# Kernel tuning notes

Measured on AMD Instinct MI355X. Metric: run time of the kernel, lower is better.

Reference implementation:

```python
import jax, jax.numpy as jnp
import numpy as np

NUM_GROUPS = 8
EPS = 1e-5


def group_norm(x, gamma, beta):
    # x: [B, C, H, W]
    B, C, H, W = x.shape
    xg = x.reshape(B, NUM_GROUPS, C // NUM_GROUPS, H, W)
    mean = xg.mean(axis=(2, 3, 4), keepdims=True)
    var = xg.var(axis=(2, 3, 4), keepdims=True)
    xn = ((xg - mean) * jax.lax.rsqrt(var + EPS)).reshape(B, C, H, W)
    return xn * gamma[None, :, None, None] + beta[None, :, None, None]


def conv1x1(x, w, b):
    # x: [B, C, H, W], w: [Cout, Cin], b: [Cout]
    return jnp.einsum('bchw,oc->bohw', x, w) + b[None, :, None, None]


def setup_inputs() -> dict:
    key = jax.random.key(0)
    ks = jax.random.split(key, 7)
    C = 128
    x = jax.random.normal(ks[0], (4, C, 64, 64), dtype=jnp.float32)
    norm_w = jnp.ones((C,), dtype=jnp.float32)
    norm_b = jnp.zeros((C,), dtype=jnp.float32)
    s = 1.0 / np.sqrt(C)
    qkv_w = jax.random.normal(ks[1], (3 * C, C), dtype=jnp.float32) * s
    qkv_b = jax.random.normal(ks[2], (3 * C,), dtype=jnp.float32) * 0.01
    proj_w = jax.random.normal(ks[3], (C, C), dtype=jnp.float32) * s
    proj_b = jax.random.normal(ks[4], (C,), dtype=jnp.float32) * 0.01
    return {"x": x, "norm_w": norm_w, "norm_b": norm_b,
            "qkv_w": qkv_w, "qkv_b": qkv_b,
            "proj_w": proj_w, "proj_b": proj_b}


def reference(x, norm_w, norm_b, qkv_w, qkv_b, proj_w, proj_b):
    B, C, H, W = x.shape
    qkv = conv1x1(group_norm(x, norm_w, norm_b), qkv_w, qkv_b)
    q, k, v = jnp.split(qkv, 3, axis=1)           # each [B, C, H, W]
    q = q.reshape(B, C, H * W).transpose(0, 2, 1)  # [B, HW, C]
    k = k.reshape(B, C, H * W)                     # [B, C, HW]
    v = v.reshape(B, C, H * W).transpose(0, 2, 1)  # [B, HW, C]
    scale = 1.0 / np.sqrt(C).astype(np.float32)
    attn = jax.nn.softmax(jnp.einsum('bnc,bcm->bnm', q, k) * scale, axis=-1)
    out = jnp.einsum('bnm,bmc->bnc', attn, v)      # [B, HW, C]
    out = out.transpose(0, 2, 1).reshape(B, C, H, W)
    return x + conv1x1(out, proj_w, proj_b)
```

## Files before the change

### kernel.cpp

```cpp
#include <hip/hip_runtime.h>

typedef unsigned short u16;
typedef unsigned int   u32;

#define HW 4096
#define NC 128

typedef __bf16 bf16x8 __attribute__((ext_vector_type(8)));
typedef float  f32x16 __attribute__((ext_vector_type(16)));

__device__ __forceinline__ bf16x8 as_bf8(uint4 u){
    union { uint4 u; bf16x8 b; } c; c.u = u; return c.b;
}
__device__ __forceinline__ u16 f2bf(float f){
    u32 u = __float_as_uint(f);
    return (u16)((u + 0x7fffu + ((u >> 16) & 1u)) >> 16);
}
__device__ __forceinline__ u32 pack2(float a, float b){
    return ((__float_as_uint(a) + 0x8000u) >> 16) | ((__float_as_uint(b) + 0x8000u) & 0xffff0000u);
}
__device__ __forceinline__ float bf_lo(u32 u){ return __uint_as_float(u << 16); }
__device__ __forceinline__ float bf_hi(u32 u){ return __uint_as_float(u & 0xffff0000u); }
__device__ __forceinline__ void unpack8(uint4 u, float* v){
    v[0]=bf_lo(u.x); v[1]=bf_hi(u.x); v[2]=bf_lo(u.y); v[3]=bf_hi(u.y);
    v[4]=bf_lo(u.z); v[5]=bf_hi(u.z); v[6]=bf_lo(u.w); v[7]=bf_hi(u.w);
}

__device__ __forceinline__ float exp2_hw(float x){ return __builtin_amdgcn_exp2f(x); }

__device__ __forceinline__ void plswap(u32 &a, u32 &b){
    asm("v_permlane32_swap_b32 %0, %1" : "+v"(a), "+v"(b));
}
__device__ __forceinline__ u32 cvtpk(float a, float b){
    u32 r; asm("v_cvt_pk_bf16_f32 %0, %1, %2" : "=v"(r) : "v"(a), "v"(b)); return r;
}

__global__ __launch_bounds__(256) void gnw_kernel(const float* __restrict__ x,
                                                  float* __restrict__ stats,
                                                  const float* __restrict__ qkv_w,
                                                  const float* __restrict__ proj_w,
                                                  uint4* __restrict__ Wf,
                                                  uint4* __restrict__ Pf){
    if (blockIdx.x < 256){
        int bg = blockIdx.x >> 3, part = blockIdx.x & 7;
        const float4* p = (const float4*)(x + (size_t)bg * 65536 + part * 8192);
        float s = 0.f, ss = 0.f;
        #pragma unroll
        for (int i = 0; i < 8; i++){
            float4 u = p[threadIdx.x + i*256];
            s  += u.x + u.y + u.z + u.w;
            ss += u.x*u.x + u.y*u.y + u.z*u.z + u.w*u.w;
        }
        #pragma unroll
        for (int off = 32; off > 0; off >>= 1){
            s  += __shfl_xor(s,  off);
            ss += __shfl_xor(ss, off);
        }
        __shared__ float rs[4], rss[4];
        int wid = threadIdx.x >> 6;
        if ((threadIdx.x & 63) == 0){ rs[wid] = s; rss[wid] = ss; }
        __syncthreads();
        if (threadIdx.x == 0){
            stats[bg*16 + part*2]     = rs[0]+rs[1]+rs[2]+rs[3];
            stats[bg*16 + part*2 + 1] = rss[0]+rss[1]+rss[2]+rss[3];
        }
    } else {
        int id = (blockIdx.x - 256)*256 + threadIdx.x;
        const float* src; uint4* dst; int fi;
        if (id < 6144){ src = qkv_w; dst = Wf; fi = id; }
        else          { src = proj_w; dst = Pf; fi = id - 6144; }
        int l = fi & 63, ks = (fi >> 6) & 7, ob = fi >> 9;
        int o = ob*32 + (l & 31);
        int c = ks*16 + ((l >> 5) << 3);
        const float* s = src + o*128 + c;
        dst[fi] = make_uint4(pack2(s[0],s[1]), pack2(s[2],s[3]), pack2(s[4],s[5]), pack2(s[6],s[7]));
    }
}

__global__ __launch_bounds__(256) void qkv_kernel(const float* __restrict__ x,
                                                  const float* __restrict__ stats,
                                                  const float* __restrict__ gamma,
                                                  const float* __restrict__ beta,
                                                  const uint4* __restrict__ Wf,
                                                  const float* __restrict__ bias,
                                                  uint4* __restrict__ Qf,
                                                  uint4* __restrict__ Kf,
                                                  uint4* __restrict__ Vf){
    __shared__ float gaL[128], beL[128], biasL[384];
    int b = blockIdx.x >> 7, tokblk = blockIdx.x & 127;
    int t = threadIdx.x, lane = t & 63, wv = t >> 6;
    if (t < 128){
        int g = t >> 4;
        float S = 0.f, SS = 0.f;
        #pragma unroll
        for (int p = 0; p < 8; p++){
            S  += stats[(b*8 + g)*16 + p*2];
            SS += stats[(b*8 + g)*16 + p*2 + 1];
        }
        float mean = S * (1.f/65536.f);
        float rstd = rsqrtf(SS * (1.f/65536.f) - mean*mean + 1e-5f);
        float ga = gamma[t] * rstd;
        gaL[t] = ga; beL[t] = beta[t] - mean*ga;
    }
    if (t < 192){ biasL[t] = bias[t]; biasL[t+192] = bias[t+192]; }
    __syncthreads();

    int h = lane >> 5, tl = lane & 31;
    uint4 xf[8];
    const float* xb = x + (size_t)b*128*HW + tokblk*32 + tl;
    #pragma unroll
    for (int ks = 0; ks < 8; ks++){
        int c0 = ks*16 + h*8;
        float4 g0 = *(float4*)&gaL[c0], g1 = *(float4*)&gaL[c0+4];
        float4 e0 = *(float4*)&beL[c0], e1 = *(float4*)&beL[c0+4];
        float v[8];
        #pragma unroll
        for (int j = 0; j < 8; j++) v[j] = xb[(size_t)(c0+j)*HW];
        v[0] = fmaf(v[0], g0.x, e0.x); v[1] = fmaf(v[1], g0.y, e0.y);
        v[2] = fmaf(v[2], g0.z, e0.z); v[3] = fmaf(v[3], g0.w, e0.w);
        v[4] = fmaf(v[4], g1.x, e1.x); v[5] = fmaf(v[5], g1.y, e1.y);
        v[6] = fmaf(v[6], g1.z, e1.z); v[7] = fmaf(v[7], g1.w, e1.w);
        xf[ks] = make_uint4(pack2(v[0],v[1]), pack2(v[2],v[3]), pack2(v[4],v[5]), pack2(v[6],v[7]));
    }

    bool up = (lane >= 32);
    #pragma unroll
    for (int i = 0; i < 3; i++){
        int ob = wv*3 + i;
        uint4 wf[8];
        #pragma unroll
        for (int ks = 0; ks < 8; ks++) wf[ks] = Wf[(ob*8 + ks)*64 + lane];
        f32x16 D;
        #pragma unroll
        for (int r = 0; r < 16; r++) D[r] = 0.f;
        if (ob < 8){
            #pragma unroll
            for (int ks = 0; ks < 8; ks++)
                D = __builtin_amdgcn_mfma_f32_32x32x16_bf16(as_bf8(wf[ks]), as_bf8(xf[ks]), D, 0,0,0);
            #pragma unroll
            for (int r = 0; r < 16; r++)
                D[r] += biasL[ob*32 + (r&3) + 8*(r>>2) + 4*h];
            u32 pk[8], xch[8];
            #pragma unroll
            for (int j = 0; j < 8; j++) pk[j] = pack2(D[2*j], D[2*j+1]);
            #pragma unroll
            for (int j = 0; j < 8; j++) xch[j] = __shfl_xor(pk[j], 32);
            uint4 F0 = up ? make_uint4(xch[2],xch[3],pk[2],pk[3]) : make_uint4(pk[0],pk[1],xch[0],xch[1]);
            uint4 F1 = up ? make_uint4(xch[6],xch[7],pk[6],pk[7]) : make_uint4(pk[4],pk[5],xch[4],xch[5]);
            uint4* dst = (ob < 4) ? Qf : Kf;
            int obl = ob & 3;
            size_t base = (((size_t)b*128 + tokblk)*8 + obl*2)*64 + lane;
            dst[base] = F0; dst[base + 64] = F1;
        } else {
            #pragma unroll
            for (int ks = 0; ks < 8; ks++)
                D = __builtin_amdgcn_mfma_f32_32x32x16_bf16(as_bf8(xf[ks]), as_bf8(wf[ks]), D, 0,0,0);
            int nb = ob - 8;
            float vb = biasL[256 + nb*32 + tl];
            #pragma unroll
            for (int r = 0; r < 16; r++) D[r] += vb;
            u32 pk[8], xch[8];
            #pragma unroll
            for (int j = 0; j < 8; j++) pk[j] = pack2(D[2*j], D[2*j+1]);
            #pragma unroll
            for (int j = 0; j < 8; j++) xch[j] = __shfl_xor(pk[j], 32);
            uint4 F0 = up ? make_uint4(xch[2],xch[3],pk[2],pk[3]) : make_uint4(pk[0],pk[1],xch[0],xch[1]);
            uint4 F1 = up ? make_uint4(xch[6],xch[7],pk[6],pk[7]) : make_uint4(pk[4],pk[5],xch[4],xch[5]);
            int it = tokblk >> 1, t2 = tokblk & 1;
            size_t base = ((((size_t)b*64 + it)*4 + nb)*4 + t2*2)*64 + lane;
            Vf[base] = F0; Vf[base + 64] = F1;
        }
    }
}

__global__ __launch_bounds__(256, 2) void attn_kernel(const uint4* __restrict__ Qf,
                                                      const uint4* __restrict__ Kf,
                                                      const uint4* __restrict__ Vf,
                                                      uint4* __restrict__ Opart,
                                                      float* __restrict__ lsum){
    __shared__ float fsm[8192];
    __shared__ float lred[64];
    int pair = blockIdx.x & 7, qx = blockIdx.x >> 3;
    int b = pair >> 1, ksp = pair & 1;
    int t = threadIdx.x, lane = t & 63, wv = t >> 6;
    int qh = wv >> 1, kh = wv & 1;
    const float SC2 = 0.12751744361402804f;
    const float B2  = -11.541560327111707f;

    uint4 qf[8];
    const uint4* qptr = Qf + (((size_t)b*128 + qx*2 + qh)*8)*64 + lane;
    #pragma unroll
    for (int ks = 0; ks < 8; ks++) qf[ks] = qptr[ks*64];

    f32x16 O[4];
    #pragma unroll
    for (int nb = 0; nb < 4; nb++)
        #pragma unroll
        for (int r = 0; r < 16; r++) O[nb][r] = 0.f;
    float l_i = 0.f;

    const uint4* kgw = Kf + (((size_t)b*128 + ksp*64)*8)*64 + (kh<<9) + lane;
    const uint4* vgw = Vf + (((size_t)b*64  + ksp*32)*16)*64 + (kh<<7) + lane;

    uint4 kf[8], vf[8];
    #pragma unroll
    for (int ks = 0; ks < 8; ks++) kf[ks] = kgw[ks*64];
    #pragma unroll
    for (int nb = 0; nb < 4; nb++){
        vf[nb*2]   = vgw[nb*256];
        vf[nb*2+1] = vgw[nb*256 + 64];
    }

    for (int it = 0; it < 32; it++){
        f32x16 Sa, Sb;
        #pragma unroll
        for (int r = 0; r < 16; r++){ Sa[r] = 0.f; Sb[r] = 0.f; }
        #pragma unroll
        for (int ks = 0; ks < 4; ks++)
            Sa = __builtin_amdgcn_mfma_f32_32x32x16_bf16(as_bf8(kf[ks]), as_bf8(qf[ks]), Sa, 0,0,0);
        #pragma unroll
        for (int ks = 4; ks < 8; ks++)
            Sb = __builtin_amdgcn_mfma_f32_32x32x16_bf16(as_bf8(kf[ks]), as_bf8(qf[ks]), Sb, 0,0,0);
        #pragma unroll
        for (int r = 0; r < 16; r++) Sa[r] += Sb[r];

        if (it < 31){
            const uint4* kn = kgw + (it+1)*1024;
            #pragma unroll
            for (int ks = 0; ks < 8; ks++) kf[ks] = kn[ks*64];
        }

        float psum = 0.f;
        u32 pk[8];
        #pragma unroll
        for (int q = 0; q < 4; q++){
            float e0 = exp2_hw(__fmaf_rn(Sa[q*4+0], SC2, B2));
            float e1 = exp2_hw(__fmaf_rn(Sa[q*4+1], SC2, B2));
            float e2 = exp2_hw(__fmaf_rn(Sa[q*4+2], SC2, B2));
            float e3 = exp2_hw(__fmaf_rn(Sa[q*4+3], SC2, B2));
            psum += (e0+e1)+(e2+e3);
            pk[2*q] = cvtpk(e0,e1); pk[2*q+1] = cvtpk(e2,e3);
        }
        {
            u32 ua = __float_as_uint(psum), ub = ua;
            plswap(ua, ub);
            l_i += __uint_as_float(ua) + __uint_as_float(ub);
        }

        plswap(pk[0], pk[2]); plswap(pk[1], pk[3]);
        plswap(pk[4], pk[6]); plswap(pk[5], pk[7]);
        uint4 fr0 = make_uint4(pk[0], pk[1], pk[2], pk[3]);
        uint4 fr1 = make_uint4(pk[4], pk[5], pk[6], pk[7]);

        #pragma unroll
        for (int nb = 0; nb < 4; nb++){
            O[nb] = __builtin_amdgcn_mfma_f32_32x32x16_bf16(as_bf8(vf[nb*2]),   as_bf8(fr0), O[nb], 0,0,0);
            O[nb] = __builtin_amdgcn_mfma_f32_32x32x16_bf16(as_bf8(vf[nb*2+1]), as_bf8(fr1), O[nb], 0,0,0);
        }

        if (it < 31){
            const uint4* vn = vgw + (it+1)*1024;
            #pragma unroll
            for (int nb = 0; nb < 4; nb++){
                vf[nb*2]   = vn[nb*256];
                vf[nb*2+1] = vn[nb*256 + 64];
            }
        }
    }

    if (kh == 1){
        #pragma unroll
        for (int nb = 0; nb < 4; nb++)
            #pragma unroll
            for (int r = 0; r < 16; r++)
                fsm[((qh*4+nb)*16 + r)*64 + lane] = O[nb][r];
        if (lane < 32) lred[qh*32 + lane] = l_i;
    }
    __syncthreads();
    if (kh == 0){
        float lt = l_i + lred[qh*32 + (lane & 31)];
        if (lane < 32) lsum[((size_t)(ksp*4 + b))*HW + (qx*2+qh)*32 + lane] = lt;
        bool up = (lane >= 32);
        uint4* oc = Opart + (size_t)ksp*262144 + (((size_t)b*128 + qx*2 + qh)*8)*64 + lane;
        #pragma unroll
        for (int nb = 0; nb < 4; nb++){
            #pragma unroll
            for (int r = 0; r < 16; r++) O[nb][r] += fsm[((qh*4+nb)*16 + r)*64 + lane];
            u32 pk[8], xch[8];
            #pragma unroll
            for (int j = 0; j < 8; j++) pk[j] = pack2(O[nb][2*j], O[nb][2*j+1]);
            #pragma unroll
            for (int j = 0; j < 8; j++) xch[j] = __shfl_xor(pk[j], 32);
            uint4 F0 = up ? make_uint4(xch[2],xch[3],pk[2],pk[3]) : make_uint4(pk[0],pk[1],xch[0],xch[1]);
            uint4 F1 = up ? make_uint4(xch[6],xch[7],pk[6],pk[7]) : make_uint4(pk[4],pk[5],xch[4],xch[5]);
            oc[(nb*2)*64]     = F0;
            oc[(nb*2 + 1)*64] = F1;
        }
    }
}

__global__ __launch_bounds__(256) void proj_kernel(const uint4* __restrict__ Op,
                                                   const float* __restrict__ lsum,
                                                   const uint4* __restrict__ Pf,
                                                   const float* __restrict__ bias,
                                                   const float* __restrict__ x,
                                                   float* __restrict__ out){
    __shared__ float biasL[128];
    int t = threadIdx.x, lane = t & 63, wv = t >> 6;
    if (t < 128) biasL[t] = bias[t];
    __syncthreads();
    int b = blockIdx.x >> 6, tk = blockIdx.x & 63;
    int tokb2 = wv & 1, obh = wv >> 1;
    int tokblk = tk*2 + tokb2;
    int h = lane >> 5, tl = lane & 31;

    int rowg = b*HW + tokblk*32 + tl;
    float inv = 1.f / (lsum[rowg] + lsum[16384 + rowg]);
    const uint4* c0p = Op + (((size_t)b*128 + tokblk)*8)*64 + lane;
    uint4 af[8];
    #pragma unroll
    for (int ks = 0; ks < 8; ks++){
        uint4 u0 = c0p[ks*64];
        uint4 u1 = c0p[262144 + ks*64];
        float v0[8], v1[8];
        unpack8(u0, v0); unpack8(u1, v1);
        u32 q[4];
        #pragma unroll
        for (int j = 0; j < 4; j++)
            q[j] = pack2((v0[2*j] + v1[2*j]) * inv, (v0[2*j+1] + v1[2*j+1]) * inv);
        af[ks] = make_uint4(q[0], q[1], q[2], q[3]);
    }

    #pragma unroll
    for (int i = 0; i < 2; i++){
        int ob = obh*2 + i;
        uint4 pf[8];
        #pragma unroll
        for (int ks = 0; ks < 8; ks++) pf[ks] = Pf[(ob*8 + ks)*64 + lane];
        f32x16 D;
        #pragma unroll
        for (int r = 0; r < 16; r++) D[r] = 0.f;
        #pragma unroll
        for (int ks = 0; ks < 8; ks++)
            D = __builtin_amdgcn_mfma_f32_32x32x16_bf16(as_bf8(pf[ks]), as_bf8(af[ks]), D, 0,0,0);
        #pragma unroll
        for (int r = 0; r < 16; r++){
            int o = ob*32 + (r&3) + 8*(r>>2) + 4*h;
            size_t gi = ((size_t)b*128 + o)*HW + tokblk*32 + tl;
            out[gi] = x[gi] + biasL[o] + D[r];
        }
    }
}

extern "C" void kernel_launch(void* const* d_in, const int* in_sizes, int n_in,
                              void* d_out, int out_size, void* d_ws, size_t ws_size,
                              hipStream_t stream){
    const float* x      = (const float*)d_in[0];
    const float* norm_w = (const float*)d_in[1];
    const float* norm_b = (const float*)d_in[2];
    const float* qkv_w  = (const float*)d_in[3];
    const float* qkv_b  = (const float*)d_in[4];
    const float* proj_w = (const float*)d_in[5];
    const float* proj_b = (const float*)d_in[6];
    float* out = (float*)d_out;

    char* w = (char*)d_ws;
    float* stats = (float*)w;
    uint4* Qf = (uint4*)(w + 2048);
    uint4* Kf = (uint4*)(w + 2048 + 4194304);
    uint4* Vf = (uint4*)(w + 2048 + 8388608);
    float* lsum = (float*)(w + 2048 + 12582912);
    uint4* Wf = (uint4*)(w + 2048 + 12582912 + 131072);
    uint4* Pf = (uint4*)(w + 2048 + 12582912 + 131072 + 98304);
    uint4* Opart = (uint4*)d_out;

    gnw_kernel<<<288, 256, 0, stream>>>(x, stats, qkv_w, proj_w, Wf, Pf);
    qkv_kernel<<<512, 256, 0, stream>>>(x, stats, norm_w, norm_b, Wf, qkv_b, Qf, Kf, Vf);
    attn_kernel<<<512, 256, 0, stream>>>(Qf, Kf, Vf, Opart, lsum);
    proj_kernel<<<256, 256, 0, stream>>>(Opart, lsum, Pf, proj_b, x, out);
}
```

Measured before the change: 130.8 us.

## Split attention keys four ways and fold partial-output merge into projection MFMAs

Templates the attention kernel on the number of key splits and, when the workspace is large enough, uses four splits with 1024 blocks, writing partial outputs to a workspace buffer. A new projection kernel sums the four unnormalized partials through MFMA accumulation (linearity of the projection) and applies the softmax normalizer afterward. This replaces the explicit bf16 unpack/add/repack. The aim is more parallelism in attention and less combine overhead. The cost is extra partial-output traffic and more projection MFMAs, and the old two-split path is kept as a fallback for small workspaces.

```diff
diff --git a/kernel.cpp b/kernel.cpp
--- a/kernel.cpp
+++ b/kernel.cpp
@@ -12,19 +12,11 @@
 __device__ __forceinline__ bf16x8 as_bf8(uint4 u){
     union { uint4 u; bf16x8 b; } c; c.u = u; return c.b;
 }
-__device__ __forceinline__ u16 f2bf(float f){
-    u32 u = __float_as_uint(f);
-    return (u16)((u + 0x7fffu + ((u >> 16) & 1u)) >> 16);
-}
 __device__ __forceinline__ u32 pack2(float a, float b){
     return ((__float_as_uint(a) + 0x8000u) >> 16) | ((__float_as_uint(b) + 0x8000u) & 0xffff0000u);
 }
 __device__ __forceinline__ float bf_lo(u32 u){ return __uint_as_float(u << 16); }
 __device__ __forceinline__ float bf_hi(u32 u){ return __uint_as_float(u & 0xffff0000u); }
-__device__ __forceinline__ void unpack8(uint4 u, float* v){
-    v[0]=bf_lo(u.x); v[1]=bf_hi(u.x); v[2]=bf_lo(u.y); v[3]=bf_hi(u.y);
-    v[4]=bf_lo(u.z); v[5]=bf_hi(u.z); v[6]=bf_lo(u.w); v[7]=bf_hi(u.w);
-}
 
 __device__ __forceinline__ float exp2_hw(float x){ return __builtin_amdgcn_exp2f(x); }
 
@@ -173,15 +165,18 @@
     }
 }
 
+template<int NS>
 __global__ __launch_bounds__(256, 2) void attn_kernel(const uint4* __restrict__ Qf,
                                                       const uint4* __restrict__ Kf,
                                                       const uint4* __restrict__ Vf,
                                                       uint4* __restrict__ Opart,
                                                       float* __restrict__ lsum){
+    constexpr int ITERS = 64 / NS;
+    constexpr int PB    = (NS == 2) ? 3 : 4;
     __shared__ float fsm[8192];
     __shared__ float lred[64];
-    int pair = blockIdx.x & 7, qx = blockIdx.x >> 3;
-    int b = pair >> 1, ksp = pair & 1;
+    int pair = blockIdx.x & ((1 << PB) - 1), qx = blockIdx.x >> PB;
+    int b = pair >> (PB - 2), ksp = pair & (NS - 1);
     int t = threadIdx.x, lane = t & 63, wv = t >> 6;
     int qh = wv >> 1, kh = wv & 1;
     const float SC2 = 0.12751744361402804f;
@@ -199,8 +194,8 @@
         for (int r = 0; r < 16; r++) O[nb][r] = 0.f;
     float l_i = 0.f;
 
-    const uint4* kgw = Kf + (((size_t)b*128 + ksp*64)*8)*64 + (kh<<9) + lane;
-    const uint4* vgw = Vf + (((size_t)b*64  + ksp*32)*16)*64 + (kh<<7) + lane;
+    const uint4* kgw = Kf + (((size_t)b*128 + ksp*(128/NS))*8)*64 + (kh<<9) + lane;
+    const uint4* vgw = Vf + (((size_t)b*64  + ksp*(64/NS))*16)*64 + (kh<<7) + lane;
 
     uint4 kf[8], vf[8];
     #pragma unroll
@@ -211,7 +206,7 @@
         vf[nb*2+1] = vgw[nb*256 + 64];
     }
 
-    for (int it = 0; it < 32; it++){
+    for (int it = 0; it < ITERS; it++){
         f32x16 Sa, Sb;
         #pragma unroll
         for (int r = 0; r < 16; r++){ Sa[r] = 0.f; Sb[r] = 0.f; }
@@ -224,7 +219,7 @@
         #pragma unroll
         for (int r = 0; r < 16; r++) Sa[r] += Sb[r];
 
-        if (it < 31){
+        if (it < ITERS-1){
             const uint4* kn = kgw + (it+1)*1024;
             #pragma unroll
             for (int ks = 0; ks < 8; ks++) kf[ks] = kn[ks*64];
@@ -258,7 +253,7 @@
             O[nb] = __builtin_amdgcn_mfma_f32_32x32x16_bf16(as_bf8(vf[nb*2+1]), as_bf8(fr1), O[nb], 0,0,0);
         }
 
-        if (it < 31){
+        if (it < ITERS-1){
             const uint4* vn = vgw + (it+1)*1024;
             #pragma unroll
             for (int nb = 0; nb < 4; nb++){
@@ -299,12 +294,12 @@
     }
 }
 
-__global__ __launch_bounds__(256) void proj_kernel(const uint4* __restrict__ Op,
-                                                   const float* __restrict__ lsum,
-                                                   const uint4* __restrict__ Pf,
-                                                   const float* __restrict__ bias,
-                                                   const float* __restrict__ x,
-                                                   float* __restrict__ out){
+__global__ __launch_bounds__(256) void proj2_kernel(const uint4* __restrict__ Op,
+                                                    const float* __restrict__ lsum,
+                                                    const uint4* __restrict__ Pf,
+                                                    const float* __restrict__ bias,
+                                                    const float* __restrict__ x,
+                                                    float* __restrict__ out){
     __shared__ float biasL[128];
     int t = threadIdx.x, lane = t & 63, wv = t >> 6;
     if (t < 128) biasL[t] = bias[t];
@@ -317,18 +312,11 @@
     int rowg = b*HW + tokblk*32 + tl;
     float inv = 1.f / (lsum[rowg] + lsum[16384 + rowg]);
     const uint4* c0p = Op + (((size_t)b*128 + tokblk)*8)*64 + lane;
-    uint4 af[8];
+    uint4 of0[8], of1[8];
     #pragma unroll
     for (int ks = 0; ks < 8; ks++){
-        uint4 u0 = c0p[ks*64];
-        uint4 u1 = c0p[262144 + ks*64];
-        float v0[8], v1[8];
-        unpack8(u0, v0); unpack8(u1, v1);
-        u32 q[4];
-        #pragma unroll
-        for (int j = 0; j < 4; j++)
-            q[j] = pack2((v0[2*j] + v1[2*j]) * inv, (v0[2*j+1] + v1[2*j+1]) * inv);
-        af[ks] = make_uint4(q[0], q[1], q[2], q[3]);
+        of0[ks] = c0p[ks*64];
+        of1[ks] = c0p[262144 + ks*64];
     }
 
     #pragma unroll
@@ -342,13 +330,60 @@
         for (int r = 0; r < 16; r++) D[r] = 0.f;
         #pragma unroll
         for (int ks = 0; ks < 8; ks++)
-            D = __builtin_amdgcn_mfma_f32_32x32x16_bf16(as_bf8(pf[ks]), as_bf8(af[ks]), D, 0,0,0);
+            D = __builtin_amdgcn_mfma_f32_32x32x16_bf16(as_bf8(pf[ks]), as_bf8(of0[ks]), D, 0,0,0);
+        #pragma unroll
+        for (int ks = 0; ks < 8; ks++)
+            D = __builtin_amdgcn_mfma_f32_32x32x16_bf16(as_bf8(pf[ks]), as_bf8(of1[ks]), D, 0,0,0);
         #pragma unroll
         for (int r = 0; r < 16; r++){
             int o = ob*32 + (r&3) + 8*(r>>2) + 4*h;
             size_t gi = ((size_t)b*128 + o)*HW + tokblk*32 + tl;
-            out[gi] = x[gi] + biasL[o] + D[r];
-        }
+            out[gi] = x[gi] + biasL[o] + D[r]*inv;
+        }
+    }
+}
+
+__global__ __launch_bounds__(256) void proj4_kernel(const uint4* __restrict__ Op,
+                                                    const float* __restrict__ lsum,
+                                                    const uint4* __restrict__ Pf,
+                                                    const float* __restrict__ bias,
+                                                    const float* __restrict__ x,
+                                                    float* __restrict__ out){
+    __shared__ float biasL[128];
+    int t = threadIdx.x, lane = t & 63, ob = t >> 6;
+    if (t < 128) biasL[t] = bias[t];
+    __syncthreads();
+    int b = blockIdx.x >> 7, tokblk = blockIdx.x & 127;
+    int h = lane >> 5, tl = lane & 31;
+    int tok = tokblk*32 + tl;
+
+    float ls = 0.f;
+    #pragma unroll
+    for (int p = 0; p < 4; p++) ls += lsum[((size_t)(p*4 + b))*HW + tok];
+    float inv = 1.f / ls;
+
+    uint4 pf[8];
+    #pragma unroll
+    for (int ks = 0; ks < 8; ks++) pf[ks] = Pf[(ob*8 + ks)*64 + lane];
+
+    const uint4* cp = Op + (((size_t)b*128 + tokblk)*8)*64 + lane;
+    f32x16 D;
+    #pragma unroll
+    for (int r = 0; r < 16; r++) D[r] = 0.f;
+    #pragma unroll
+    for (int c = 0; c < 4; c++){
+        uint4 of[8];
+        #pragma unroll
+        for (int ks = 0; ks < 8; ks++) of[ks] = cp[(size_t)c*262144 + ks*64];
+        #pragma unroll
+        for (int ks = 0; ks < 8; ks++)
+            D = __builtin_amdgcn_mfma_f32_32x32x16_bf16(as_bf8(pf[ks]), as_bf8(of[ks]), D, 0,0,0);
+    }
+    #pragma unroll
+    for (int r = 0; r < 16; r++){
+        int o = ob*32 + (r&3) + 8*(r>>2) + 4*h;
+        size_t gi = ((size_t)b*128 + o)*HW + tokblk*32 + tl;
+        out[gi] = x[gi] + biasL[o] + D[r]*inv;
     }
 }
 
@@ -363,19 +398,36 @@
     const float* proj_w = (const float*)d_in[5];
     const float* proj_b = (const float*)d_in[6];
     float* out = (float*)d_out;
-
     char* w = (char*)d_ws;
-    float* stats = (float*)w;
-    uint4* Qf = (uint4*)(w + 2048);
-    uint4* Kf = (uint4*)(w + 2048 + 4194304);
-    uint4* Vf = (uint4*)(w + 2048 + 8388608);
-    float* lsum = (float*)(w + 2048 + 12582912);
-    uint4* Wf = (uint4*)(w + 2048 + 12582912 + 131072);
-    uint4* Pf = (uint4*)(w + 2048 + 12582912 + 131072 + 98304);
-    uint4* Opart = (uint4*)d_out;
-
-    gnw_kernel<<<288, 256, 0, stream>>>(x, stats, qkv_w, proj_w, Wf, Pf);
-    qkv_kernel<<<512, 256, 0, stream>>>(x, stats, norm_w, norm_b, Wf, qkv_b, Qf, Kf, Vf);
-    attn_kernel<<<512, 256, 0, stream>>>(Qf, Kf, Vf, Opart, lsum);
-    proj_kernel<<<256, 256, 0, stream>>>(Opart, lsum, Pf, proj_b, x, out);
-}
+
+    const size_t needA = 2048 + 3*4194304 + 262144 + 98304 + 32768 + 16777216;
+    if (ws_size >= needA){
+        float* stats = (float*)w;
+        uint4* Qf   = (uint4*)(w + 2048);
+        uint4* Kf   = (uint4*)(w + 2048 + 4194304);
+        uint4* Vf   = (uint4*)(w + 2048 + 8388608);
+        float* lsum = (float*)(w + 12584960);
+        uint4* Wf   = (uint4*)(w + 12847104);
+        uint4* Pf   = (uint4*)(w + 12945408);
+        uint4* Op4  = (uint4*)(w + 12978176);
+
+        gnw_kernel<<<288, 256, 0, stream>>>(x, stats, qkv_w, proj_w, Wf, Pf);
+        qkv_kernel<<<512, 256, 0, stream>>>(x, stats, norm_w, norm_b, Wf, qkv_b, Qf, Kf, Vf);
+        attn_kernel<4><<<1024, 256, 0, stream>>>(Qf, Kf, Vf, Op4, lsum);
+        proj4_kernel<<<512, 256, 0, stream>>>(Op4, lsum, Pf, proj_b, x, out);
+    } else {
+        float* stats = (float*)w;
+        uint4* Qf   = (uint4*)(w + 2048);
+        uint4* Kf   = (uint4*)(w + 2048 + 4194304);
+        uint4* Vf   = (uint4*)(w + 2048 + 8388608);
+        float* lsum = (float*)(w + 2048 + 12582912);
+        uint4* Wf   = (uint4*)(w + 2048 + 12582912 + 131072);
+        uint4* Pf   = (uint4*)(w + 2048 + 12582912 + 131072 + 98304);
+        uint4* Opart = (uint4*)d_out;
+
+        gnw_kernel<<<288, 256, 0, stream>>>(x, stats, qkv_w, proj_w, Wf, Pf);
+        qkv_kernel<<<512, 256, 0, stream>>>(x, stats, norm_w, norm_b, Wf, qkv_b, Qf, Kf, Vf);
+        attn_kernel<2><<<512, 256, 0, stream>>>(Qf, Kf, Vf, Opart, lsum);
+        proj2_kernel<<<256, 256, 0, stream>>>(Opart, lsum, Pf, proj_b, x, out);
+    }
+}
```

Measured after the change: 131.1 us. About the same (+0.2%).
